# Kernel tuning notes

Hardware: AMD Instinct MI355X
Metric: run time of the kernel (lower is better)

## Reference

```python
import jax, jax.numpy as jnp
import numpy as np

N_NODES = 100000
N_EDGES = 1600000
IN_FEAT = 128
OUT_FEAT = 128


def setup_inputs() -> dict:
    key = jax.random.key(0)
    k1, k2, k3 = jax.random.split(key, 3)
    x = jax.random.normal(k1, (N_NODES, IN_FEAT), dtype=jnp.float32)
    W = jax.random.normal(k2, (IN_FEAT, OUT_FEAT), dtype=jnp.float32) * (1.0 / np.sqrt(IN_FEAT))
    b = jnp.zeros((OUT_FEAT,), dtype=jnp.float32)
    edge_index = jax.random.randint(k3, (2, N_EDGES), 0, N_NODES, dtype=jnp.int64)
    return {"x": x, "W": W, "b": b, "edge_index": edge_index}


def reference(x, W, b, edge_index):
    # PyG GCNConv: add self-loops, symmetric deg normalization, scatter-add.
    N = x.shape[0]
    loops = jnp.arange(N, dtype=edge_index.dtype)
    ei = jnp.concatenate([edge_index, jnp.stack([loops, loops])], axis=1)  # [2, E+N]
    row, col = ei[0], ei[1]  # source, target
    ones = jnp.ones(ei.shape[1], dtype=x.dtype)
    deg = jax.ops.segment_sum(ones, col, num_segments=N)  # in-degree incl. self-loop
    deg_inv_sqrt = jnp.where(deg > 0, jax.lax.rsqrt(deg), 0.0)
    norm = deg_inv_sqrt[row] * deg_inv_sqrt[col]  # [E+N]
    xw = x @ W  # [N, out_feat]
    msg = xw[row] * norm[:, None]  # gather + normalize
    out = jax.ops.segment_sum(msg, col, num_segments=N) + b  # scatter-add + bias
    return out
```

## Files before the change

kernel.cpp:

```cpp
#include <hip/hip_runtime.h>

#define N_NODES 100000
#define N_EDGES 1600000
#define FEAT 128
#define NBUCK 782
#define BUCK_SHIFT 7
#define BUCK_MASK 127
#define HIST_EPB 4096
#define HIST_BLOCKS 391
#define SCAT_BLOCKS 391
#define GEMM_BLOCKS 782
#define WT_PITCH 136
#define MAX_BUCK 3072

typedef __attribute__((ext_vector_type(8))) short short8;
typedef __attribute__((ext_vector_type(4))) float f32x4;
typedef __attribute__((ext_vector_type(2))) float f32x2;

__device__ inline unsigned short f2bf(float f) {
    unsigned u = __builtin_bit_cast(unsigned, f);
    unsigned r = (u + 0x7FFFu + ((u >> 16) & 1u)) >> 16;
    return (unsigned short)r;
}
__device__ inline float bf2f(unsigned h) {
    unsigned u = h << 16;
    return __builtin_bit_cast(float, u);
}
__device__ inline unsigned pkbf(float a, float b) {
    return (unsigned)f2bf(a) | ((unsigned)f2bf(b) << 16);
}

__global__ __launch_bounds__(256)
void k_hist_wt(const int* __restrict__ col, int* __restrict__ bcnt,
               const float* __restrict__ W, unsigned short* __restrict__ Wt) {
    int bid = blockIdx.x, tid = threadIdx.x;
    if (bid == HIST_BLOCKS) {
        for (int idx = tid; idx < FEAT * FEAT; idx += 256) {
            int k = idx >> 7, n = idx & 127;
            Wt[n * WT_PITCH + k] = f2bf(W[idx]);
        }
        return;
    }
    __shared__ int hist[NBUCK];
    for (int i = tid; i < NBUCK; i += 256) hist[i] = 0;
    __syncthreads();
    int e0 = bid * HIST_EPB;
    int n = min(HIST_EPB, N_EDGES - e0);
    for (int i = tid * 4; i < n; i += 1024) {
        if (i + 3 < n) {
            int4 c4 = *(const int4*)(col + e0 + i);
            atomicAdd(&hist[c4.x >> BUCK_SHIFT], 1);
            atomicAdd(&hist[c4.y >> BUCK_SHIFT], 1);
            atomicAdd(&hist[c4.z >> BUCK_SHIFT], 1);
            atomicAdd(&hist[c4.w >> BUCK_SHIFT], 1);
        } else {
            for (int j = i; j < n; ++j) atomicAdd(&hist[col[e0 + j] >> BUCK_SHIFT], 1);
        }
    }
    __syncthreads();
    for (int i = tid; i < NBUCK; i += 256) {
        int h = hist[i];
        if (h) atomicAdd(&bcnt[i], h);
    }
}

__global__ __launch_bounds__(1024)
void k_bscan(const int* __restrict__ bcnt, int* __restrict__ bstarts,
             int* __restrict__ bcursor) {
    __shared__ int s[1024];
    int tid = threadIdx.x;
    int v = (tid < NBUCK) ? bcnt[tid] : 0;
    s[tid] = v;
    __syncthreads();
    for (int off = 1; off < 1024; off <<= 1) {
        int t = (tid >= off) ? s[tid - off] : 0;
        __syncthreads();
        s[tid] += t;
        __syncthreads();
    }
    if (tid < NBUCK) {
        int ex = s[tid] - v;
        bstarts[tid] = ex;
        bcursor[tid] = ex;
    }
    if (tid == NBUCK - 1) bstarts[NBUCK] = s[tid];
}

__global__ __launch_bounds__(256)
void k_scatter_gemm(const int* __restrict__ row, const int* __restrict__ col,
                    int* __restrict__ bcursor, unsigned* __restrict__ ebuf,
                    const float* __restrict__ x, const unsigned short* __restrict__ Wt,
                    unsigned short* __restrict__ yb) {
    __shared__ union U {
        struct { int hist[NBUCK]; int gbase[NBUCK]; } sc;
        unsigned short ws[18432];
    } u;
    int bid = blockIdx.x, tid = threadIdx.x;

    if (bid < SCAT_BLOCKS) {
        for (int i = tid; i < NBUCK; i += 256) u.sc.hist[i] = 0;
        __syncthreads();
        int e0 = bid * HIST_EPB;
        int n = min(HIST_EPB, N_EDGES - e0);
        for (int i = tid * 4; i < n; i += 1024) {
            if (i + 3 < n) {
                int4 c4 = *(const int4*)(col + e0 + i);
                atomicAdd(&u.sc.hist[c4.x >> BUCK_SHIFT], 1);
                atomicAdd(&u.sc.hist[c4.y >> BUCK_SHIFT], 1);
                atomicAdd(&u.sc.hist[c4.z >> BUCK_SHIFT], 1);
                atomicAdd(&u.sc.hist[c4.w >> BUCK_SHIFT], 1);
            } else {
                for (int j = i; j < n; ++j) atomicAdd(&u.sc.hist[col[e0 + j] >> BUCK_SHIFT], 1);
            }
        }
        __syncthreads();
        for (int i = tid; i < NBUCK; i += 256) {
            int h = u.sc.hist[i];
            u.sc.gbase[i] = h ? atomicAdd(&bcursor[i], h) : 0;
        }
        __syncthreads();
        for (int i = tid; i < NBUCK; i += 256) u.sc.hist[i] = 0;
        __syncthreads();
        for (int i = tid * 4; i < n; i += 1024) {
            if (i + 3 < n) {
                int4 c4 = *(const int4*)(col + e0 + i);
                int4 r4 = *(const int4*)(row + e0 + i);
                int bk, off;
                bk = c4.x >> BUCK_SHIFT; off = atomicAdd(&u.sc.hist[bk], 1);
                ebuf[u.sc.gbase[bk] + off] = ((unsigned)r4.x << BUCK_SHIFT) | (unsigned)(c4.x & BUCK_MASK);
                bk = c4.y >> BUCK_SHIFT; off = atomicAdd(&u.sc.hist[bk], 1);
                ebuf[u.sc.gbase[bk] + off] = ((unsigned)r4.y << BUCK_SHIFT) | (unsigned)(c4.y & BUCK_MASK);
                bk = c4.z >> BUCK_SHIFT; off = atomicAdd(&u.sc.hist[bk], 1);
                ebuf[u.sc.gbase[bk] + off] = ((unsigned)r4.z << BUCK_SHIFT) | (unsigned)(c4.z & BUCK_MASK);
                bk = c4.w >> BUCK_SHIFT; off = atomicAdd(&u.sc.hist[bk], 1);
                ebuf[u.sc.gbase[bk] + off] = ((unsigned)r4.w << BUCK_SHIFT) | (unsigned)(c4.w & BUCK_MASK);
            } else {
                for (int j = i; j < n; ++j) {
                    int c = col[e0 + j], r = row[e0 + j];
                    int bk = c >> BUCK_SHIFT;
                    int off = atomicAdd(&u.sc.hist[bk], 1);
                    ebuf[u.sc.gbase[bk] + off] = ((unsigned)r << BUCK_SHIFT) | (unsigned)(c & BUCK_MASK);
                }
            }
        }
        return;
    }

    int gb = bid - SCAT_BLOCKS;
    for (int i = tid; i < 2304; i += 256)
        ((uint4*)u.ws)[i] = ((const uint4*)Wt)[i];
    __syncthreads();

    int lane = tid & 63, wv = tid >> 6;
    int m = lane & 15, quad = lane >> 4;
    int rowT0 = gb * 128 + wv * 32;
    int ar0 = rowT0 + m;       if (ar0 >= N_NODES) ar0 = N_NODES - 1;
    int ar1 = rowT0 + 16 + m;  if (ar1 >= N_NODES) ar1 = N_NODES - 1;
    const float* xr0 = x + (size_t)ar0 * FEAT + quad * 8;
    const float* xr1 = x + (size_t)ar1 * FEAT + quad * 8;

    f32x4 acc[2][8];
#pragma unroll
    for (int t = 0; t < 2; ++t)
#pragma unroll
        for (int nt = 0; nt < 8; ++nt) acc[t][nt] = (f32x4){0.f, 0.f, 0.f, 0.f};

#pragma unroll
    for (int kk = 0; kk < 4; ++kk) {
        float4 a0 = *(const float4*)(xr0 + kk * 32);
        float4 a1 = *(const float4*)(xr0 + kk * 32 + 4);
        float4 b0 = *(const float4*)(xr1 + kk * 32);
        float4 b1 = *(const float4*)(xr1 + kk * 32 + 4);
        union { unsigned w[4]; short8 v; } A0, A1;
        A0.w[0] = pkbf(a0.x, a0.y); A0.w[1] = pkbf(a0.z, a0.w);
        A0.w[2] = pkbf(a1.x, a1.y); A0.w[3] = pkbf(a1.z, a1.w);
        A1.w[0] = pkbf(b0.x, b0.y); A1.w[1] = pkbf(b0.z, b0.w);
        A1.w[2] = pkbf(b1.x, b1.y); A1.w[3] = pkbf(b1.z, b1.w);
        const unsigned short* wp = u.ws + m * WT_PITCH + kk * 32 + quad * 8;
#pragma unroll
        for (int nt = 0; nt < 8; ++nt) {
            short8 bf = *(const short8*)(wp + nt * 16 * WT_PITCH);
            acc[0][nt] = __builtin_amdgcn_mfma_f32_16x16x32_bf16(A0.v, bf, acc[0][nt], 0, 0, 0);
            acc[1][nt] = __builtin_amdgcn_mfma_f32_16x16x32_bf16(A1.v, bf, acc[1][nt], 0, 0, 0);
        }
    }

#pragma unroll
    for (int t = 0; t < 2; ++t) {
        int r0 = rowT0 + t * 16 + quad * 4;
#pragma unroll
        for (int nt = 0; nt < 8; ++nt) {
            int cc = nt * 16 + m;
#pragma unroll
            for (int r = 0; r < 4; ++r) {
                int rr = r0 + r;
                if (rr < N_NODES) yb[(size_t)rr * FEAT + cc] = f2bf(acc[t][nt][r]);
            }
        }
    }
}

__global__ __launch_bounds__(256)
void k_dinv(const unsigned* __restrict__ ebuf, const int* __restrict__ bstarts,
            float* __restrict__ dinv) {
    __shared__ int hist[128];
    int b = blockIdx.x, tid = threadIdx.x;
    if (tid < 128) hist[tid] = 0;
    __syncthreads();
    int e0 = bstarts[b], e1 = bstarts[b + 1];
    for (int i = e0 + tid; i < e1; i += 256) atomicAdd(&hist[ebuf[i] & BUCK_MASK], 1);
    __syncthreads();
    int node0 = b << BUCK_SHIFT;
    if (tid < 128 && node0 + tid < N_NODES)
        dinv[node0 + tid] = rsqrtf((float)(hist[tid] + 1));
}

__global__ __launch_bounds__(256)
void k_agg(const unsigned short* __restrict__ yb, const unsigned* __restrict__ ebuf,
           const int* __restrict__ bstarts, const float* __restrict__ dinv,
           const float* __restrict__ bias, float* __restrict__ out) {
    __shared__ unsigned elist[MAX_BUCK];
    __shared__ int slist[MAX_BUCK];
    __shared__ int hist[128], sstart[128], cur[128];
    __shared__ float dloc[128];
    int b = blockIdx.x, tid = threadIdx.x;
    int node0 = b << BUCK_SHIFT;
    if (tid < 128) hist[tid] = 0;
    __syncthreads();
    int e0 = bstarts[b];
    int ne = bstarts[b + 1] - e0;
    if (ne > MAX_BUCK) ne = MAX_BUCK;
    for (int i = tid; i < ne; i += 256) {
        unsigned e = ebuf[e0 + i];
        elist[i] = e;
        atomicAdd(&hist[e & BUCK_MASK], 1);
    }
    __syncthreads();
    if (tid < 128) sstart[tid] = hist[tid];
    __syncthreads();
    for (int off = 1; off < 128; off <<= 1) {
        int t = 0;
        if (tid < 128 && tid >= off) t = sstart[tid - off];
        __syncthreads();
        if (tid < 128) sstart[tid] += t;
        __syncthreads();
    }
    if (tid < 128) {
        int ex = sstart[tid] - hist[tid];
        sstart[tid] = ex;
        cur[tid] = ex;
        dloc[tid] = rsqrtf((float)(hist[tid] + 1));
    }
    __syncthreads();
    for (int i = tid; i < ne; i += 256) {
        unsigned e = elist[i];
        int t = e & BUCK_MASK;
        int p = atomicAdd(&cur[t], 1);
        slist[p] = (int)(e >> BUCK_SHIFT);
    }
    __syncthreads();

    int wv = tid >> 6, lane = tid & 63;
    const unsigned* y1 = (const unsigned*)yb;
    float2 bb = ((const float2*)bias)[lane];
    for (int nl = wv; nl < 128; nl += 4) {
        int node = node0 + nl;
        if (node >= N_NODES) break;
        float di = dloc[nl];
        unsigned sv = y1[(size_t)node * 64 + lane];
        float a0 = di * bf2f(sv & 0xFFFFu);
        float a1 = di * bf2f(sv >> 16);
        int st = sstart[nl], deg = hist[nl];
        for (int base = 0; base < deg; base += 64) {
            int nn = min(64, deg - base);
            int src = 0;
            float dv = 0.f;
            if (lane < nn) {
                src = slist[st + base + lane];
                dv = dinv[src];
            }
            int j = 0;
            for (; j + 3 < nn; j += 4) {
                int s0 = __shfl(src, j),     s1 = __shfl(src, j + 1);
                int s2 = __shfl(src, j + 2), s3 = __shfl(src, j + 3);
                float d0 = __shfl(dv, j),     d1 = __shfl(dv, j + 1);
                float d2 = __shfl(dv, j + 2), d3 = __shfl(dv, j + 3);
                unsigned v0 = y1[(size_t)s0 * 64 + lane];
                unsigned v1 = y1[(size_t)s1 * 64 + lane];
                unsigned v2 = y1[(size_t)s2 * 64 + lane];
                unsigned v3 = y1[(size_t)s3 * 64 + lane];
                a0 += d0 * bf2f(v0 & 0xFFFFu); a1 += d0 * bf2f(v0 >> 16);
                a0 += d1 * bf2f(v1 & 0xFFFFu); a1 += d1 * bf2f(v1 >> 16);
                a0 += d2 * bf2f(v2 & 0xFFFFu); a1 += d2 * bf2f(v2 >> 16);
                a0 += d3 * bf2f(v3 & 0xFFFFu); a1 += d3 * bf2f(v3 >> 16);
            }
            for (; j < nn; ++j) {
                int s = __shfl(src, j);
                float d = __shfl(dv, j);
                unsigned v = y1[(size_t)s * 64 + lane];
                a0 += d * bf2f(v & 0xFFFFu);
                a1 += d * bf2f(v >> 16);
            }
        }
        f32x2 o;
        o.x = bb.x + di * a0;
        o.y = bb.y + di * a1;
        __builtin_nontemporal_store(o, (f32x2*)(out + (size_t)node * FEAT) + lane);
    }
}

extern "C" void kernel_launch(void* const* d_in, const int* in_sizes, int n_in,
                              void* d_out, int out_size, void* d_ws, size_t ws_size,
                              hipStream_t stream) {
    const float* x = (const float*)d_in[0];
    const float* W = (const float*)d_in[1];
    const float* b = (const float*)d_in[2];
    const int* ei = (const int*)d_in[3];
    const int* row = ei;
    const int* col = ei + N_EDGES;
    float* out = (float*)d_out;

    char* ws = (char*)d_ws;
    size_t off = 0;
    auto alloc = [&](size_t bytes) -> void* {
        void* p = ws + off;
        off += (bytes + 511) & ~(size_t)511;
        return p;
    };
    int* bcnt          = (int*)alloc((NBUCK + 1) * 4);
    int* bstarts       = (int*)alloc((NBUCK + 1) * 4);
    int* bcursor       = (int*)alloc((NBUCK + 1) * 4);
    float* dinv        = (float*)alloc((size_t)N_NODES * 4);
    unsigned* ebuf     = (unsigned*)alloc((size_t)N_EDGES * 4);
    unsigned short* Wt = (unsigned short*)alloc(36864);
    unsigned short* yb = (unsigned short*)alloc((size_t)N_NODES * FEAT * 2);

    (void)hipMemsetAsync(bcnt, 0, (NBUCK + 1) * 4, stream);

    k_hist_wt<<<HIST_BLOCKS + 1, 256, 0, stream>>>(col, bcnt, W, Wt);
    k_bscan<<<1, 1024, 0, stream>>>(bcnt, bstarts, bcursor);
    k_scatter_gemm<<<SCAT_BLOCKS + GEMM_BLOCKS, 256, 0, stream>>>(
        row, col, bcursor, ebuf, x, Wt, yb);
    k_dinv<<<NBUCK, 256, 0, stream>>>(ebuf, bstarts, dinv);
    k_agg<<<NBUCK, 256, 0, stream>>>(yb, ebuf, bstarts, dinv, b, out);
}
```

Before: 272.4 us.

## Replace histogram+scan bucketing with fixed-capacity buckets via global atomics

Drops the separate histogram pass, the bucket prefix scan and the memset. Edges are now placed into fixed-size per-bucket slots (MAX_BUCK each) using one global atomic per edge. The GEMM now reads W directly from global/L1 instead of staging it in LDS, and k_agg reads edges from global memory twice instead of caching them in LDS. This cuts two kernel launches and one pass over col, but adds heavy global atomic contention and silently drops edges if a bucket overflows its capacity.

```diff
diff --git a/kernel.cpp b/kernel.cpp
--- a/kernel.cpp
+++ b/kernel.cpp
@@ -6,12 +6,10 @@
 #define NBUCK 782
 #define BUCK_SHIFT 7
 #define BUCK_MASK 127
-#define HIST_EPB 4096
-#define HIST_BLOCKS 391
+#define MAX_BUCK 3072
+#define GEMM_BLOCKS 782
+#define SCAT_EPB 4096
 #define SCAT_BLOCKS 391
-#define GEMM_BLOCKS 782
-#define WT_PITCH 136
-#define MAX_BUCK 3072
 
 typedef __attribute__((ext_vector_type(8))) short short8;
 typedef __attribute__((ext_vector_type(4))) float f32x4;
@@ -31,129 +29,57 @@
 }
 
 __global__ __launch_bounds__(256)
-void k_hist_wt(const int* __restrict__ col, int* __restrict__ bcnt,
-               const float* __restrict__ W, unsigned short* __restrict__ Wt) {
-    int bid = blockIdx.x, tid = threadIdx.x;
-    if (bid == HIST_BLOCKS) {
+void k_pre(int* __restrict__ bcnt, const float* __restrict__ W,
+           unsigned short* __restrict__ Wt) {
+    int tid = threadIdx.x;
+    if (blockIdx.x == 0) {
+        for (int i = tid; i < NBUCK; i += 256) bcnt[i] = 0;
+    } else {
         for (int idx = tid; idx < FEAT * FEAT; idx += 256) {
             int k = idx >> 7, n = idx & 127;
-            Wt[n * WT_PITCH + k] = f2bf(W[idx]);
-        }
-        return;
-    }
-    __shared__ int hist[NBUCK];
-    for (int i = tid; i < NBUCK; i += 256) hist[i] = 0;
-    __syncthreads();
-    int e0 = bid * HIST_EPB;
-    int n = min(HIST_EPB, N_EDGES - e0);
-    for (int i = tid * 4; i < n; i += 1024) {
-        if (i + 3 < n) {
-            int4 c4 = *(const int4*)(col + e0 + i);
-            atomicAdd(&hist[c4.x >> BUCK_SHIFT], 1);
-            atomicAdd(&hist[c4.y >> BUCK_SHIFT], 1);
-            atomicAdd(&hist[c4.z >> BUCK_SHIFT], 1);
-            atomicAdd(&hist[c4.w >> BUCK_SHIFT], 1);
-        } else {
-            for (int j = i; j < n; ++j) atomicAdd(&hist[col[e0 + j] >> BUCK_SHIFT], 1);
-        }
-    }
-    __syncthreads();
-    for (int i = tid; i < NBUCK; i += 256) {
-        int h = hist[i];
-        if (h) atomicAdd(&bcnt[i], h);
-    }
-}
-
-__global__ __launch_bounds__(1024)
-void k_bscan(const int* __restrict__ bcnt, int* __restrict__ bstarts,
-             int* __restrict__ bcursor) {
-    __shared__ int s[1024];
-    int tid = threadIdx.x;
-    int v = (tid < NBUCK) ? bcnt[tid] : 0;
-    s[tid] = v;
-    __syncthreads();
-    for (int off = 1; off < 1024; off <<= 1) {
-        int t = (tid >= off) ? s[tid - off] : 0;
-        __syncthreads();
-        s[tid] += t;
-        __syncthreads();
-    }
-    if (tid < NBUCK) {
-        int ex = s[tid] - v;
-        bstarts[tid] = ex;
-        bcursor[tid] = ex;
-    }
-    if (tid == NBUCK - 1) bstarts[NBUCK] = s[tid];
-}
-
-__global__ __launch_bounds__(256)
-void k_scatter_gemm(const int* __restrict__ row, const int* __restrict__ col,
-                    int* __restrict__ bcursor, unsigned* __restrict__ ebuf,
-                    const float* __restrict__ x, const unsigned short* __restrict__ Wt,
-                    unsigned short* __restrict__ yb) {
-    __shared__ union U {
-        struct { int hist[NBUCK]; int gbase[NBUCK]; } sc;
-        unsigned short ws[18432];
-    } u;
+            Wt[n * FEAT + k] = f2bf(W[idx]);
+        }
+    }
+}
+
+__global__ __launch_bounds__(256)
+void k_gemm_scatter(const float* __restrict__ x, const unsigned short* __restrict__ Wt,
+                    unsigned short* __restrict__ yb,
+                    const int* __restrict__ row, const int* __restrict__ col,
+                    int* __restrict__ bcnt, unsigned* __restrict__ ebuf) {
     int bid = blockIdx.x, tid = threadIdx.x;
 
-    if (bid < SCAT_BLOCKS) {
-        for (int i = tid; i < NBUCK; i += 256) u.sc.hist[i] = 0;
-        __syncthreads();
-        int e0 = bid * HIST_EPB;
-        int n = min(HIST_EPB, N_EDGES - e0);
-        for (int i = tid * 4; i < n; i += 1024) {
-            if (i + 3 < n) {
-                int4 c4 = *(const int4*)(col + e0 + i);
-                atomicAdd(&u.sc.hist[c4.x >> BUCK_SHIFT], 1);
-                atomicAdd(&u.sc.hist[c4.y >> BUCK_SHIFT], 1);
-                atomicAdd(&u.sc.hist[c4.z >> BUCK_SHIFT], 1);
-                atomicAdd(&u.sc.hist[c4.w >> BUCK_SHIFT], 1);
-            } else {
-                for (int j = i; j < n; ++j) atomicAdd(&u.sc.hist[col[e0 + j] >> BUCK_SHIFT], 1);
-            }
-        }
-        __syncthreads();
-        for (int i = tid; i < NBUCK; i += 256) {
-            int h = u.sc.hist[i];
-            u.sc.gbase[i] = h ? atomicAdd(&bcursor[i], h) : 0;
-        }
-        __syncthreads();
-        for (int i = tid; i < NBUCK; i += 256) u.sc.hist[i] = 0;
-        __syncthreads();
+    if (bid >= GEMM_BLOCKS) {
+        int e0 = (bid - GEMM_BLOCKS) * SCAT_EPB;
+        int n = min(SCAT_EPB, N_EDGES - e0);
         for (int i = tid * 4; i < n; i += 1024) {
             if (i + 3 < n) {
                 int4 c4 = *(const int4*)(col + e0 + i);
                 int4 r4 = *(const int4*)(row + e0 + i);
-                int bk, off;
-                bk = c4.x >> BUCK_SHIFT; off = atomicAdd(&u.sc.hist[bk], 1);
-                ebuf[u.sc.gbase[bk] + off] = ((unsigned)r4.x << BUCK_SHIFT) | (unsigned)(c4.x & BUCK_MASK);
-                bk = c4.y >> BUCK_SHIFT; off = atomicAdd(&u.sc.hist[bk], 1);
-                ebuf[u.sc.gbase[bk] + off] = ((unsigned)r4.y << BUCK_SHIFT) | (unsigned)(c4.y & BUCK_MASK);
-                bk = c4.z >> BUCK_SHIFT; off = atomicAdd(&u.sc.hist[bk], 1);
-                ebuf[u.sc.gbase[bk] + off] = ((unsigned)r4.z << BUCK_SHIFT) | (unsigned)(c4.z & BUCK_MASK);
-                bk = c4.w >> BUCK_SHIFT; off = atomicAdd(&u.sc.hist[bk], 1);
-                ebuf[u.sc.gbase[bk] + off] = ((unsigned)r4.w << BUCK_SHIFT) | (unsigned)(c4.w & BUCK_MASK);
+                int bk, pos;
+                bk = c4.x >> BUCK_SHIFT; pos = atomicAdd(&bcnt[bk], 1);
+                if (pos < MAX_BUCK) ebuf[bk * MAX_BUCK + pos] = ((unsigned)r4.x << BUCK_SHIFT) | (unsigned)(c4.x & BUCK_MASK);
+                bk = c4.y >> BUCK_SHIFT; pos = atomicAdd(&bcnt[bk], 1);
+                if (pos < MAX_BUCK) ebuf[bk * MAX_BUCK + pos] = ((unsigned)r4.y << BUCK_SHIFT) | (unsigned)(c4.y & BUCK_MASK);
+                bk = c4.z >> BUCK_SHIFT; pos = atomicAdd(&bcnt[bk], 1);
+                if (pos < MAX_BUCK) ebuf[bk * MAX_BUCK + pos] = ((unsigned)r4.z << BUCK_SHIFT) | (unsigned)(c4.z & BUCK_MASK);
+                bk = c4.w >> BUCK_SHIFT; pos = atomicAdd(&bcnt[bk], 1);
+                if (pos < MAX_BUCK) ebuf[bk * MAX_BUCK + pos] = ((unsigned)r4.w << BUCK_SHIFT) | (unsigned)(c4.w & BUCK_MASK);
             } else {
                 for (int j = i; j < n; ++j) {
                     int c = col[e0 + j], r = row[e0 + j];
                     int bk = c >> BUCK_SHIFT;
-                    int off = atomicAdd(&u.sc.hist[bk], 1);
-                    ebuf[u.sc.gbase[bk] + off] = ((unsigned)r << BUCK_SHIFT) | (unsigned)(c & BUCK_MASK);
+                    int pos = atomicAdd(&bcnt[bk], 1);
+                    if (pos < MAX_BUCK) ebuf[bk * MAX_BUCK + pos] = ((unsigned)r << BUCK_SHIFT) | (unsigned)(c & BUCK_MASK);
                 }
             }
         }
         return;
     }
-
-    int gb = bid - SCAT_BLOCKS;
-    for (int i = tid; i < 2304; i += 256)
-        ((uint4*)u.ws)[i] = ((const uint4*)Wt)[i];
-    __syncthreads();
 
     int lane = tid & 63, wv = tid >> 6;
     int m = lane & 15, quad = lane >> 4;
-    int rowT0 = gb * 128 + wv * 32;
+    int rowT0 = bid * 128 + wv * 32;
     int ar0 = rowT0 + m;       if (ar0 >= N_NODES) ar0 = N_NODES - 1;
     int ar1 = rowT0 + 16 + m;  if (ar1 >= N_NODES) ar1 = N_NODES - 1;
     const float* xr0 = x + (size_t)ar0 * FEAT + quad * 8;
@@ -176,10 +102,10 @@
         A0.w[2] = pkbf(a1.x, a1.y); A0.w[3] = pkbf(a1.z, a1.w);
         A1.w[0] = pkbf(b0.x, b0.y); A1.w[1] = pkbf(b0.z, b0.w);
         A1.w[2] = pkbf(b1.x, b1.y); A1.w[3] = pkbf(b1.z, b1.w);
-        const unsigned short* wp = u.ws + m * WT_PITCH + kk * 32 + quad * 8;
+        const unsigned short* wp = Wt + m * FEAT + kk * 32 + quad * 8;
 #pragma unroll
         for (int nt = 0; nt < 8; ++nt) {
-            short8 bf = *(const short8*)(wp + nt * 16 * WT_PITCH);
+            short8 bf = *(const short8*)(wp + nt * 16 * FEAT);
             acc[0][nt] = __builtin_amdgcn_mfma_f32_16x16x32_bf16(A0.v, bf, acc[0][nt], 0, 0, 0);
             acc[1][nt] = __builtin_amdgcn_mfma_f32_16x16x32_bf16(A1.v, bf, acc[1][nt], 0, 0, 0);
         }
@@ -201,14 +127,15 @@
 }
 
 __global__ __launch_bounds__(256)
-void k_dinv(const unsigned* __restrict__ ebuf, const int* __restrict__ bstarts,
+void k_dinv(const unsigned* __restrict__ ebuf, const int* __restrict__ bcnt,
             float* __restrict__ dinv) {
     __shared__ int hist[128];
     int b = blockIdx.x, tid = threadIdx.x;
     if (tid < 128) hist[tid] = 0;
     __syncthreads();
-    int e0 = bstarts[b], e1 = bstarts[b + 1];
-    for (int i = e0 + tid; i < e1; i += 256) atomicAdd(&hist[ebuf[i] & BUCK_MASK], 1);
+    int ne = min(bcnt[b], MAX_BUCK);
+    const unsigned* eb = ebuf + (size_t)b * MAX_BUCK;
+    for (int i = tid; i < ne; i += 256) atomicAdd(&hist[eb[i] & BUCK_MASK], 1);
     __syncthreads();
     int node0 = b << BUCK_SHIFT;
     if (tid < 128 && node0 + tid < N_NODES)
@@ -217,24 +144,19 @@
 
 __global__ __launch_bounds__(256)
 void k_agg(const unsigned short* __restrict__ yb, const unsigned* __restrict__ ebuf,
-           const int* __restrict__ bstarts, const float* __restrict__ dinv,
+           const int* __restrict__ bcnt, const float* __restrict__ dinv,
            const float* __restrict__ bias, float* __restrict__ out) {
-    __shared__ unsigned elist[MAX_BUCK];
     __shared__ int slist[MAX_BUCK];
     __shared__ int hist[128], sstart[128], cur[128];
     __shared__ float dloc[128];
     int b = blockIdx.x, tid = threadIdx.x;
     int node0 = b << BUCK_SHIFT;
+    int ne = min(bcnt[b], MAX_BUCK);
+    const unsigned* eb = ebuf + (size_t)b * MAX_BUCK;
+
     if (tid < 128) hist[tid] = 0;
     __syncthreads();
-    int e0 = bstarts[b];
-    int ne = bstarts[b + 1] - e0;
-    if (ne > MAX_BUCK) ne = MAX_BUCK;
-    for (int i = tid; i < ne; i += 256) {
-        unsigned e = ebuf[e0 + i];
-        elist[i] = e;
-        atomicAdd(&hist[e & BUCK_MASK], 1);
-    }
+    for (int i = tid; i < ne; i += 256) atomicAdd(&hist[eb[i] & BUCK_MASK], 1);
     __syncthreads();
     if (tid < 128) sstart[tid] = hist[tid];
     __syncthreads();
@@ -253,9 +175,8 @@
     }
     __syncthreads();
     for (int i = tid; i < ne; i += 256) {
-        unsigned e = elist[i];
-        int t = e & BUCK_MASK;
-        int p = atomicAdd(&cur[t], 1);
+        unsigned e = eb[i];
+        int p = atomicAdd(&cur[e & BUCK_MASK], 1);
         slist[p] = (int)(e >> BUCK_SHIFT);
     }
     __syncthreads();
@@ -327,20 +248,15 @@
         off += (bytes + 511) & ~(size_t)511;
         return p;
     };
-    int* bcnt          = (int*)alloc((NBUCK + 1) * 4);
-    int* bstarts       = (int*)alloc((NBUCK + 1) * 4);
-    int* bcursor       = (int*)alloc((NBUCK + 1) * 4);
+    int* bcnt          = (int*)alloc(NBUCK * 4);
     float* dinv        = (float*)alloc((size_t)N_NODES * 4);
-    unsigned* ebuf     = (unsigned*)alloc((size_t)N_EDGES * 4);
-    unsigned short* Wt = (unsigned short*)alloc(36864);
+    unsigned* ebuf     = (unsigned*)alloc((size_t)NBUCK * MAX_BUCK * 4);
+    unsigned short* Wt = (unsigned short*)alloc((size_t)FEAT * FEAT * 2);
     unsigned short* yb = (unsigned short*)alloc((size_t)N_NODES * FEAT * 2);
 
-    (void)hipMemsetAsync(bcnt, 0, (NBUCK + 1) * 4, stream);
-
-    k_hist_wt<<<HIST_BLOCKS + 1, 256, 0, stream>>>(col, bcnt, W, Wt);
-    k_bscan<<<1, 1024, 0, stream>>>(bcnt, bstarts, bcursor);
-    k_scatter_gemm<<<SCAT_BLOCKS + GEMM_BLOCKS, 256, 0, stream>>>(
-        row, col, bcursor, ebuf, x, Wt, yb);
-    k_dinv<<<NBUCK, 256, 0, stream>>>(ebuf, bstarts, dinv);
-    k_agg<<<NBUCK, 256, 0, stream>>>(yb, ebuf, bstarts, dinv, b, out);
-}
+    k_pre<<<2, 256, 0, stream>>>(bcnt, W, Wt);
+    k_gemm_scatter<<<GEMM_BLOCKS + SCAT_BLOCKS, 256, 0, stream>>>(
+        x, Wt, yb, row, col, bcnt, ebuf);
+    k_dinv<<<NBUCK, 256, 0, stream>>>(ebuf, bcnt, dinv);
+    k_agg<<<NBUCK, 256, 0, stream>>>(yb, ebuf, bcnt, dinv, b, out);
+}
```

Result: slower. 607.8 us (+123.1%).
